# Kernel tuning notes

Hardware: AMD Instinct MI355X
Metric: run time of the kernel (lower is better)

## Reference

```python
import jax, jax.numpy as jnp
import numpy as np

ITEM_NUM = 50000
MAXLEN = 128
D_MODEL = 64
D_STATE = 32
D_CONV = 4
EXPAND = 2
D_INNER = EXPAND * D_MODEL  # 128
DT_RANK = max(1, -(-D_MODEL // 16))  # ceil(64/16) = 4
STD = 0.02


def setup_inputs() -> dict:
    key = jax.random.key(0)
    ks = jax.random.split(key, 12)
    B, L = 32, MAXLEN
    input_ids = jax.random.randint(ks[0], (B, L), 0, ITEM_NUM + 1)
    item_emb = STD * jax.random.normal(ks[1], (ITEM_NUM + 1, D_MODEL), jnp.float32)
    item_emb = item_emb.at[0].set(0.0)  # padding_idx=0 zeroed
    pos_emb = STD * jax.random.normal(ks[2], (MAXLEN, D_MODEL), jnp.float32)
    in_proj_w = STD * jax.random.normal(ks[3], (2 * D_INNER, D_MODEL), jnp.float32)
    conv_w = STD * jax.random.normal(ks[4], (D_INNER, D_CONV), jnp.float32)
    conv_b = jnp.zeros((D_INNER,), jnp.float32)
    x_proj_w = STD * jax.random.normal(ks[5], (DT_RANK + 2 * D_STATE, D_INNER), jnp.float32)
    dt_proj_w = STD * jax.random.normal(ks[6], (D_INNER, DT_RANK), jnp.float32)
    dt_proj_b = jnp.zeros((D_INNER,), jnp.float32)
    # A initialized as log of 1..d_state broadcast over channels (mamba_ssm S4D-real init)
    A_log = jnp.log(jnp.broadcast_to(jnp.arange(1, D_STATE + 1, dtype=jnp.float32), (D_INNER, D_STATE)))
    D_param = jnp.ones((D_INNER,), jnp.float32)
    out_proj_w = STD * jax.random.normal(ks[7], (D_MODEL, D_INNER), jnp.float32)
    return dict(input_ids=input_ids, item_emb=item_emb, pos_emb=pos_emb,
                in_proj_w=in_proj_w, conv_w=conv_w, conv_b=conv_b,
                x_proj_w=x_proj_w, dt_proj_w=dt_proj_w, dt_proj_b=dt_proj_b,
                A_log=A_log, D_param=D_param, out_proj_w=out_proj_w)


def _mamba_block(x, in_proj_w, conv_w, conv_b, x_proj_w, dt_proj_w, dt_proj_b, A_log, D_param, out_proj_w):
    B, L, _ = x.shape
    xz = jnp.einsum('bld,ed->ble', x, in_proj_w)  # (B,L,2*D_INNER)
    xc, z = jnp.split(xz, 2, axis=-1)
    # causal depthwise conv1d, kernel D_CONV, left-pad D_CONV-1
    xp = jnp.pad(xc, ((0, 0), (D_CONV - 1, 0), (0, 0)))
    xc = sum(xp[:, k:k + L, :] * conv_w[:, k] for k in range(D_CONV)) + conv_b
    xc = jax.nn.silu(xc)
    dbl = jnp.einsum('blc,ec->ble', xc, x_proj_w)
    dt, Bm, Cm = jnp.split(dbl, [DT_RANK, DT_RANK + D_STATE], axis=-1)
    delta = jax.nn.softplus(jnp.einsum('blr,cr->blc', dt, dt_proj_w) + dt_proj_b)  # (B,L,D_INNER)
    A = -jnp.exp(A_log)  # (D_INNER, D_STATE)
    dA = jnp.exp(delta[..., None] * A)                       # (B,L,C,S)
    dBu = delta[..., None] * Bm[:, :, None, :] * xc[..., None]  # (B,L,C,S)

    def step(h, inp):
        dA_t, dBu_t, C_t = inp  # (B,C,S),(B,C,S),(B,S)
        h = dA_t * h + dBu_t
        y = jnp.einsum('bcs,bs->bc', h, C_t)
        return h, y

    h0 = jnp.zeros((B, D_INNER, D_STATE), xc.dtype)
    _, ys = jax.lax.scan(step, h0, (dA.transpose(1, 0, 2, 3), dBu.transpose(1, 0, 2, 3), Cm.transpose(1, 0, 2)))
    y = ys.transpose(1, 0, 2) + D_param * xc  # (B,L,D_INNER)
    y = y * jax.nn.silu(z)
    return jnp.einsum('blc,dc->bld', y, out_proj_w)


def reference(input_ids, item_emb, pos_emb, in_proj_w, conv_w, conv_b,
              x_proj_w, dt_proj_w, dt_proj_b, A_log, D_param, out_proj_w):
    B, L = input_ids.shape
    seqs = item_emb[input_ids] * (D_MODEL ** 0.5)
    seqs = seqs + pos_emb[jnp.arange(L)][None, :, :]
    # dropout is identity in eval/deterministic mode
    pad_mask = (input_ids == 0)
    seqs = jnp.where(pad_mask[..., None], 0.0, seqs)
    seqs = _mamba_block(seqs, in_proj_w, conv_w, conv_b, x_proj_w,
                        dt_proj_w, dt_proj_b, A_log, D_param, out_proj_w)
    logits = jnp.einsum('bld,vd->blv', seqs, item_emb)  # matmul with item_emb.T
    return logits
```

## Files before the change

kernel.cpp:

```cpp
#include <hip/hip_runtime.h>
#include <math.h>

#define BB 32
#define LL 128
#define DM 64
#define DI 128
#define NV 50001
#define BL (BB*LL)
#define TM 32
#define TN 512
#define NT2 98
#define NPAD2 (NT2*TN)

typedef float f32x4 __attribute__((ext_vector_type(4)));
typedef _Float16 h16x8 __attribute__((ext_vector_type(8)));

__device__ __forceinline__ float silu_f(float x) { return x / (1.0f + expf(-x)); }

__global__ __launch_bounds__(512, 1) void k_pre(
    const int* __restrict__ ids, const float* __restrict__ item_emb,
    const float* __restrict__ pos_emb, const float* __restrict__ in_proj_w,
    const float* __restrict__ conv_w, const float* __restrict__ conv_b,
    const float* __restrict__ x_proj_w, const float* __restrict__ dt_proj_w,
    const float* __restrict__ dt_proj_b,
    float* __restrict__ zs_g, float* __restrict__ xcs_g,
    float* __restrict__ dbl_g, float* __restrict__ delta_g) {
    __shared__ float sq[67 * 68];
    __shared__ float px[67 * 132];
    __shared__ float cvS[64 * 132];
    __shared__ float dblS[64 * 68];
    const int t = threadIdx.x;
    const int bb = blockIdx.x >> 1, half = blockIdx.x & 1;
    const int l0 = half * 64;

    {
        int d = t & 63;
        for (int i = t >> 6; i < 67; i += 8) {
            int tl = l0 - 3 + i;
            float v = 0.f;
            if (tl >= 0) {
                int id = ids[bb * LL + tl];
                if (id != 0) v = item_emb[id * DM + d] * 8.0f + pos_emb[tl * DM + d];
            }
            sq[i * 68 + d] = v;
        }
    }
    __syncthreads();
    {
        int r = t & 63;
        int q = __builtin_amdgcn_readfirstlane(t >> 6);
        f32x4 s4[16];
        #pragma unroll
        for (int k = 0; k < 16; k++) s4[k] = *(const f32x4*)&sq[r * 68 + 4 * k];
        float acc[32];
        #pragma unroll
        for (int j = 0; j < 32; j++) acc[j] = 0.f;
        const float* wq = in_proj_w + (q * 32) * DM;
        #pragma unroll 4
        for (int j = 0; j < 32; j++) {
            float a = 0.f;
            #pragma unroll
            for (int k = 0; k < 16; k++) {
                f32x4 w4 = *(const f32x4*)&wq[j * DM + 4 * k];
                a += s4[k].x * w4.x + s4[k].y * w4.y + s4[k].z * w4.z + s4[k].w * w4.w;
            }
            acc[j] = a;
        }
        int tok = l0 - 3 + r;
        if (q < 4) {
            #pragma unroll
            for (int j4 = 0; j4 < 8; j4++) {
                f32x4 v = {acc[4 * j4], acc[4 * j4 + 1], acc[4 * j4 + 2], acc[4 * j4 + 3]};
                *(f32x4*)&px[r * 132 + q * 32 + 4 * j4] = v;
            }
        } else if (tok >= 0) {
            float* dst = zs_g + (size_t)(bb * LL + tok) * DI + (q - 4) * 32;
            #pragma unroll
            for (int j = 0; j < 32; j++) dst[j] = silu_f(acc[j]);
        }
    }
    __syncthreads();
    {
        int e = t & 255;
        for (int hr = 64 + (t >> 8); hr < 67; hr += 2) {
            float a = 0.f;
            const float* w = in_proj_w + e * DM;
            #pragma unroll
            for (int k = 0; k < 16; k++) {
                f32x4 sv = *(const f32x4*)&sq[hr * 68 + 4 * k];
                f32x4 wv = *(const f32x4*)&w[4 * k];
                a += sv.x * wv.x + sv.y * wv.y + sv.z * wv.z + sv.w * wv.w;
            }
            int tok = l0 - 3 + hr;
            if (e < 128) px[hr * 132 + e] = a;
            else zs_g[(size_t)(bb * LL + tok) * DI + (e - 128)] = silu_f(a);
        }
    }
    __syncthreads();
    {
        int c = t & 127, r4 = t >> 7;
        float cw0 = conv_w[c * 4], cw1 = conv_w[c * 4 + 1];
        float cw2 = conv_w[c * 4 + 2], cw3 = conv_w[c * 4 + 3];
        float cb = conv_b[c];
        for (int g = 0; g < 16; g++) {
            int j = 4 * g + r4;
            float x0 = px[j * 132 + c], x1 = px[(j + 1) * 132 + c];
            float x2 = px[(j + 2) * 132 + c], x3 = px[(j + 3) * 132 + c];
            float v = silu_f(cb + x0 * cw0 + x1 * cw1 + x2 * cw2 + x3 * cw3);
            cvS[j * 132 + c] = v;
            xcs_g[(size_t)(bb * LL + l0 + j) * DI + c] = v;
        }
    }
    __syncthreads();
    {
        int r = t & 63;
        int q = __builtin_amdgcn_readfirstlane(t >> 6);
        int e0 = q * 9;
        float acc[9];
        #pragma unroll
        for (int j = 0; j < 9; j++) acc[j] = 0.f;
        #pragma unroll
        for (int kc = 0; kc < 4; kc++) {
            f32x4 xr[8];
            #pragma unroll
            for (int k4 = 0; k4 < 8; k4++)
                xr[k4] = *(const f32x4*)&cvS[r * 132 + kc * 32 + 4 * k4];
            #pragma unroll
            for (int j = 0; j < 9; j++) {
                int e = e0 + j;
                if (e < 68) {
                    const float* w = x_proj_w + (size_t)e * DI + kc * 32;
                    float a = acc[j];
                    #pragma unroll
                    for (int k4 = 0; k4 < 8; k4++) {
                        f32x4 wv = *(const f32x4*)&w[4 * k4];
                        a += xr[k4].x * wv.x + xr[k4].y * wv.y + xr[k4].z * wv.z + xr[k4].w * wv.w;
                    }
                    acc[j] = a;
                }
            }
        }
        int row = bb * LL + l0 + r;
        #pragma unroll
        for (int j = 0; j < 9; j++) {
            int e = e0 + j;
            if (e < 68) {
                dblS[r * 68 + e] = acc[j];
                if (e >= 4) dbl_g[(size_t)row * 64 + (e - 4)] = acc[j];
            }
        }
    }
    __syncthreads();
    {
        int r = t & 63;
        int q = __builtin_amdgcn_readfirstlane(t >> 6);
        f32x4 dt = *(const f32x4*)&dblS[r * 68];
        int row = bb * LL + l0 + r;
        #pragma unroll
        for (int j = 0; j < 16; j++) {
            int c = q * 16 + j;
            float a = dt_proj_b[c] + dt.x * dt_proj_w[c * 4] + dt.y * dt_proj_w[c * 4 + 1]
                    + dt.z * dt_proj_w[c * 4 + 2] + dt.w * dt_proj_w[c * 4 + 3];
            float sp = (a > 20.f) ? a : log1pf(expf(a));
            delta_g[(size_t)row * DI + c] = sp;
        }
    }
}

__global__ __launch_bounds__(512, 1) void k_scan(
    const float* __restrict__ delta_g, const float* __restrict__ xcs_g,
    const float* __restrict__ dbl_g, const float* __restrict__ zs_g,
    const float* __restrict__ A_log, const float* __restrict__ Dp,
    float* __restrict__ y_g) {
    const int t = threadIdx.x;
    const int b = blockIdx.x >> 3, ce = blockIdx.x & 7;
    const int grp = t >> 5, s = t & 31;
    const int c = ce * 16 + grp;
    const size_t r0 = (size_t)(b * LL);
    float Acs = -expf(A_log[c * 32 + s]);
    float Dc = Dp[c];
    float h = 0.f;
    float Bt = dbl_g[r0 * 64 + s], Ct = dbl_g[r0 * 64 + 32 + s];
    float dlt = delta_g[r0 * DI + c], xct = xcs_g[r0 * DI + c];
    float zt = zs_g[r0 * DI + c];
    for (int tt = 0; tt < LL; tt++) {
        float Bn = 0.f, Cn = 0.f, zn = 0.f, dn = 0.f, xn = 0.f;
        if (tt < LL - 1) {
            size_t rn = r0 + tt + 1;
            Bn = dbl_g[rn * 64 + s]; Cn = dbl_g[rn * 64 + 32 + s];
            dn = delta_g[rn * DI + c]; xn = xcs_g[rn * DI + c];
            zn = zs_g[rn * DI + c];
        }
        h = expf(dlt * Acs) * h + (dlt * Bt) * xct;
        float p = h * Ct;
        #pragma unroll
        for (int off = 16; off; off >>= 1) p += __shfl_xor(p, off, 32);
        if (s == 0) y_g[(r0 + tt) * DI + c] = (p + Dc * xct) * zt;
        dlt = dn; xct = xn; Bt = Bn; Ct = Cn; zt = zn;
    }
}

__global__ void k_outproj(const float* __restrict__ y, const float* __restrict__ w,
                          _Float16* __restrict__ outp_h) {
    int row = blockIdx.x;
    int d = threadIdx.x;
    __shared__ float ys[DI];
    ys[d] = y[(size_t)row * DI + d];
    ys[d + 64] = y[(size_t)row * DI + d + 64];
    __syncthreads();
    float acc = 0.f;
    const float* wr = w + d * DI;
    #pragma unroll
    for (int c = 0; c < DI; c++) acc += ys[c] * wr[c];
    outp_h[(size_t)row * 64 + d] = (_Float16)(acc * 262144.0f);
}

__global__ void k_cvt_emb(const float* __restrict__ emb, _Float16* __restrict__ embh) {
    int i = blockIdx.x * 256 + threadIdx.x;
    int r = i >> 6, d = i & 63;
    float v = (r < NV) ? emb[(size_t)r * 64 + d] * 1024.0f : 0.f;
    embh[i] = (_Float16)v;
}

__global__ __launch_bounds__(256, 2) void k_logits(
    const _Float16* __restrict__ A, const _Float16* __restrict__ Bm,
    float* __restrict__ logits) {
    __shared__ _Float16 As[TM * 72];
    __shared__ _Float16 Bs[TN * 72];
    const int m0 = blockIdx.x * TM;
    const int n0 = blockIdx.y * TN;
    const int t = threadIdx.x;

    {
        int r = t >> 3, c8 = t & 7;
        *(h16x8*)&As[r * 72 + c8 * 8] = *(const h16x8*)&A[(size_t)(m0 + r) * 64 + c8 * 8];
    }
    #pragma unroll
    for (int q = 0; q < 16; q++) {
        int idx = t + q * 256;
        int r = idx >> 3, c8 = idx & 7;
        *(h16x8*)&Bs[r * 72 + c8 * 8] = *(const h16x8*)&Bm[(size_t)(n0 + r) * 64 + c8 * 8];
    }
    __syncthreads();

    const int lane = t & 63, wv = t >> 6;
    const int lr = lane & 15, lg = lane >> 4;
    f32x4 acc[2][8];
    #pragma unroll
    for (int mi = 0; mi < 2; mi++)
        #pragma unroll
        for (int ni = 0; ni < 8; ni++)
            acc[mi][ni] = f32x4{0.f, 0.f, 0.f, 0.f};

    #pragma unroll
    for (int step = 0; step < 2; step++) {
        int kb = step * 32 + lg * 8;
        h16x8 a[2], b[8];
        #pragma unroll
        for (int mi = 0; mi < 2; mi++)
            a[mi] = *(const h16x8*)&As[(16 * mi + lr) * 72 + kb];
        #pragma unroll
        for (int ni = 0; ni < 8; ni++)
            b[ni] = *(const h16x8*)&Bs[(128 * wv + 16 * ni + lr) * 72 + kb];
        #pragma unroll
        for (int mi = 0; mi < 2; mi++)
            #pragma unroll
            for (int ni = 0; ni < 8; ni++)
                acc[mi][ni] = __builtin_amdgcn_mfma_f32_16x16x32_f16(a[mi], b[ni], acc[mi][ni], 0, 0, 0);
    }
    __syncthreads();

    float* Cs = (float*)Bs;
    const float SC = 3.7252902984619140625e-09f;
    #pragma unroll
    for (int mi = 0; mi < 2; mi++)
        #pragma unroll
        for (int ni = 0; ni < 8; ni++) {
            int col = 128 * wv + 16 * ni + lr;
            #pragma unroll
            for (int j = 0; j < 4; j++) {
                int row = 16 * mi + 4 * lg + j;
                Cs[row * 517 + col] = acc[mi][ni][j] * SC;
            }
        }
    __syncthreads();

    #pragma unroll
    for (int q = 0; q < 16; q++) {
        int r = 2 * q + (t >> 7);
        int c = t & 127;
        int grow = m0 + r;
        int s = (4 - (grow & 3)) & 3;
        float* dst = logits + (size_t)grow * NV + n0;
        const float* src = Cs + r * 517;
        if (s == 0) {
            int col = 4 * c;
            int gc = n0 + col;
            if (gc + 3 < NV) {
                __builtin_nontemporal_store(*(const f32x4*)&src[col], (f32x4*)&dst[col]);
            } else {
                #pragma unroll
                for (int e = 0; e < 4; e++)
                    if (gc + e < NV) __builtin_nontemporal_store(src[col + e], &dst[col + e]);
            }
        } else {
            if (c == 0) {
                for (int e = 0; e < s; e++)
                    if (n0 + e < NV) __builtin_nontemporal_store(src[e], &dst[e]);
            }
            if (c < 127) {
                int col = s + 4 * c;
                int gc = n0 + col;
                if (gc + 3 < NV) {
                    __builtin_nontemporal_store(*(const f32x4*)&src[col], (f32x4*)&dst[col]);
                } else {
                    #pragma unroll
                    for (int e = 0; e < 4; e++)
                        if (gc + e < NV) __builtin_nontemporal_store(src[col + e], &dst[col + e]);
                }
            } else {
                for (int e = s + 508; e < 512; e++)
                    if (n0 + e < NV) __builtin_nontemporal_store(src[e], &dst[e]);
            }
        }
    }
}

extern "C" void kernel_launch(void* const* d_in, const int* in_sizes, int n_in,
                              void* d_out, int out_size, void* d_ws, size_t ws_size,
                              hipStream_t stream) {
    const int*   ids       = (const int*)  d_in[0];
    const float* item_emb  = (const float*)d_in[1];
    const float* pos_emb   = (const float*)d_in[2];
    const float* in_proj_w = (const float*)d_in[3];
    const float* conv_w    = (const float*)d_in[4];
    const float* conv_b    = (const float*)d_in[5];
    const float* x_proj_w  = (const float*)d_in[6];
    const float* dt_proj_w = (const float*)d_in[7];
    const float* dt_proj_b = (const float*)d_in[8];
    const float* A_log     = (const float*)d_in[9];
    const float* Dp        = (const float*)d_in[10];
    const float* out_proj_w= (const float*)d_in[11];
    float* logits = (float*)d_out;

    float* ws     = (float*)d_ws;
    float* zs     = ws;
    float* xcs    = zs + (size_t)BL * DI;
    float* dblg   = xcs + (size_t)BL * DI;
    float* deltag = dblg + (size_t)BL * 64;
    float* yg     = deltag + (size_t)BL * DI;
    _Float16* outph = (_Float16*)(yg + (size_t)BL * DI);
    _Float16* embh  = outph + (size_t)BL * 64;

    k_cvt_emb<<<(NPAD2 * 64) / 256, 256, 0, stream>>>(item_emb, embh);
    k_pre<<<64, 512, 0, stream>>>(ids, item_emb, pos_emb, in_proj_w, conv_w, conv_b,
                                  x_proj_w, dt_proj_w, dt_proj_b,
                                  zs, xcs, dblg, deltag);
    k_scan<<<256, 512, 0, stream>>>(deltag, xcs, dblg, zs, A_log, Dp, yg);
    k_outproj<<<BL, 64, 0, stream>>>(yg, out_proj_w, outph);
    dim3 lgd(BL / TM, NT2);
    k_logits<<<lgd, 256, 0, stream>>>(outph, embh, logits);
}
```

Before: 412.7 us.

## Split preprocessing into 16-token tiles and batch out-projection rows per block

k_pre now runs 256 blocks, each handling 16 tokens with a 3-token halo, instead of 64 blocks of 64 tokens. The GEMV loops are restructured so each thread keeps a weight row in registers and streams activations from shared memory. k_outproj processes 8 rows per 256-thread block with weights held in registers and vectorised loads, replacing one tiny block per row. The intent is more parallelism across CUs and less launch and weight-reload overhead, at the cost of redundant halo recomputation and higher register pressure.

```diff
diff --git a/kernel.cpp b/kernel.cpp
--- a/kernel.cpp
+++ b/kernel.cpp
@@ -25,18 +25,18 @@
     const float* __restrict__ dt_proj_b,
     float* __restrict__ zs_g, float* __restrict__ xcs_g,
     float* __restrict__ dbl_g, float* __restrict__ delta_g) {
-    __shared__ float sq[67 * 68];
-    __shared__ float px[67 * 132];
-    __shared__ float cvS[64 * 132];
-    __shared__ float dblS[64 * 68];
+    __shared__ float sq[19 * 68];
+    __shared__ float px[19 * 132];
+    __shared__ float cvS[16 * 132];
+    __shared__ float dtS[16 * 4];
     const int t = threadIdx.x;
-    const int bb = blockIdx.x >> 1, half = blockIdx.x & 1;
-    const int l0 = half * 64;
+    const int bb = blockIdx.x >> 3, e8 = blockIdx.x & 7;
+    const int T0 = e8 * 16;
 
     {
         int d = t & 63;
-        for (int i = t >> 6; i < 67; i += 8) {
-            int tl = l0 - 3 + i;
+        for (int i = t >> 6; i < 19; i += 8) {
+            int tl = T0 - 3 + i;
             float v = 0.f;
             if (tl >= 0) {
                 int id = ids[bb * LL + tl];
@@ -47,122 +47,82 @@
     }
     __syncthreads();
     {
-        int r = t & 63;
-        int q = __builtin_amdgcn_readfirstlane(t >> 6);
-        f32x4 s4[16];
-        #pragma unroll
-        for (int k = 0; k < 16; k++) s4[k] = *(const f32x4*)&sq[r * 68 + 4 * k];
-        float acc[32];
-        #pragma unroll
-        for (int j = 0; j < 32; j++) acc[j] = 0.f;
-        const float* wq = in_proj_w + (q * 32) * DM;
-        #pragma unroll 4
-        for (int j = 0; j < 32; j++) {
+        int e = t & 255, half = t >> 8;
+        f32x4 w4[16];
+        const float* wr = in_proj_w + e * DM;
+        #pragma unroll
+        for (int k = 0; k < 16; k++) w4[k] = *(const f32x4*)&wr[4 * k];
+        int i0 = half ? 10 : 0, i1 = half ? 19 : 10;
+        for (int i = i0; i < i1; i++) {
             float a = 0.f;
             #pragma unroll
             for (int k = 0; k < 16; k++) {
-                f32x4 w4 = *(const f32x4*)&wq[j * DM + 4 * k];
-                a += s4[k].x * w4.x + s4[k].y * w4.y + s4[k].z * w4.z + s4[k].w * w4.w;
-            }
-            acc[j] = a;
-        }
-        int tok = l0 - 3 + r;
-        if (q < 4) {
-            #pragma unroll
-            for (int j4 = 0; j4 < 8; j4++) {
-                f32x4 v = {acc[4 * j4], acc[4 * j4 + 1], acc[4 * j4 + 2], acc[4 * j4 + 3]};
-                *(f32x4*)&px[r * 132 + q * 32 + 4 * j4] = v;
-            }
-        } else if (tok >= 0) {
-            float* dst = zs_g + (size_t)(bb * LL + tok) * DI + (q - 4) * 32;
-            #pragma unroll
-            for (int j = 0; j < 32; j++) dst[j] = silu_f(acc[j]);
-        }
-    }
-    __syncthreads();
-    {
-        int e = t & 255;
-        for (int hr = 64 + (t >> 8); hr < 67; hr += 2) {
-            float a = 0.f;
-            const float* w = in_proj_w + e * DM;
-            #pragma unroll
-            for (int k = 0; k < 16; k++) {
-                f32x4 sv = *(const f32x4*)&sq[hr * 68 + 4 * k];
-                f32x4 wv = *(const f32x4*)&w[4 * k];
-                a += sv.x * wv.x + sv.y * wv.y + sv.z * wv.z + sv.w * wv.w;
-            }
-            int tok = l0 - 3 + hr;
-            if (e < 128) px[hr * 132 + e] = a;
-            else zs_g[(size_t)(bb * LL + tok) * DI + (e - 128)] = silu_f(a);
-        }
-    }
-    __syncthreads();
-    {
-        int c = t & 127, r4 = t >> 7;
+                f32x4 s = *(const f32x4*)&sq[i * 68 + 4 * k];
+                a += s.x * w4[k].x + s.y * w4[k].y + s.z * w4[k].z + s.w * w4[k].w;
+            }
+            if (e < 128) px[i * 132 + e] = a;
+            else if (i >= 3) zs_g[(size_t)(bb * LL + T0 + i - 3) * DI + (e - 128)] = silu_f(a);
+        }
+    }
+    __syncthreads();
+    {
+        int c = t & 127;
         float cw0 = conv_w[c * 4], cw1 = conv_w[c * 4 + 1];
         float cw2 = conv_w[c * 4 + 2], cw3 = conv_w[c * 4 + 3];
         float cb = conv_b[c];
-        for (int g = 0; g < 16; g++) {
-            int j = 4 * g + r4;
-            float x0 = px[j * 132 + c], x1 = px[(j + 1) * 132 + c];
-            float x2 = px[(j + 2) * 132 + c], x3 = px[(j + 3) * 132 + c];
-            float v = silu_f(cb + x0 * cw0 + x1 * cw1 + x2 * cw2 + x3 * cw3);
+        #pragma unroll
+        for (int m = 0; m < 4; m++) {
+            int j = 4 * m + (t >> 7);
+            float v = silu_f(cb + px[j * 132 + c] * cw0 + px[(j + 1) * 132 + c] * cw1
+                                + px[(j + 2) * 132 + c] * cw2 + px[(j + 3) * 132 + c] * cw3);
             cvS[j * 132 + c] = v;
-            xcs_g[(size_t)(bb * LL + l0 + j) * DI + c] = v;
-        }
-    }
-    __syncthreads();
-    {
-        int r = t & 63;
-        int q = __builtin_amdgcn_readfirstlane(t >> 6);
-        int e0 = q * 9;
-        float acc[9];
-        #pragma unroll
-        for (int j = 0; j < 9; j++) acc[j] = 0.f;
-        #pragma unroll
-        for (int kc = 0; kc < 4; kc++) {
-            f32x4 xr[8];
-            #pragma unroll
-            for (int k4 = 0; k4 < 8; k4++)
-                xr[k4] = *(const f32x4*)&cvS[r * 132 + kc * 32 + 4 * k4];
-            #pragma unroll
-            for (int j = 0; j < 9; j++) {
-                int e = e0 + j;
-                if (e < 68) {
-                    const float* w = x_proj_w + (size_t)e * DI + kc * 32;
-                    float a = acc[j];
-                    #pragma unroll
-                    for (int k4 = 0; k4 < 8; k4++) {
-                        f32x4 wv = *(const f32x4*)&w[4 * k4];
-                        a += xr[k4].x * wv.x + xr[k4].y * wv.y + xr[k4].z * wv.z + xr[k4].w * wv.w;
-                    }
-                    acc[j] = a;
-                }
-            }
-        }
-        int row = bb * LL + l0 + r;
-        #pragma unroll
-        for (int j = 0; j < 9; j++) {
-            int e = e0 + j;
-            if (e < 68) {
-                dblS[r * 68 + e] = acc[j];
-                if (e >= 4) dbl_g[(size_t)row * 64 + (e - 4)] = acc[j];
-            }
-        }
-    }
-    __syncthreads();
-    {
-        int r = t & 63;
-        int q = __builtin_amdgcn_readfirstlane(t >> 6);
-        f32x4 dt = *(const f32x4*)&dblS[r * 68];
-        int row = bb * LL + l0 + r;
-        #pragma unroll
-        for (int j = 0; j < 16; j++) {
-            int c = q * 16 + j;
-            float a = dt_proj_b[c] + dt.x * dt_proj_w[c * 4] + dt.y * dt_proj_w[c * 4 + 1]
-                    + dt.z * dt_proj_w[c * 4 + 2] + dt.w * dt_proj_w[c * 4 + 3];
+            xcs_g[(size_t)(bb * LL + T0 + j) * DI + c] = v;
+        }
+    }
+    __syncthreads();
+    {
+        int e = 4 + (t & 63), jg = t >> 6;
+        f32x4 w4[32];
+        const float* wr = x_proj_w + (size_t)e * DI;
+        #pragma unroll
+        for (int k = 0; k < 32; k++) w4[k] = *(const f32x4*)&wr[4 * k];
+        #pragma unroll
+        for (int jj = 0; jj < 2; jj++) {
+            int j = jg + 8 * jj;
+            float a = 0.f;
+            #pragma unroll
+            for (int k = 0; k < 32; k++) {
+                f32x4 x = *(const f32x4*)&cvS[j * 132 + 4 * k];
+                a += x.x * w4[k].x + x.y * w4[k].y + x.z * w4[k].z + x.w * w4[k].w;
+            }
+            dbl_g[(size_t)(bb * LL + T0 + j) * 64 + (e - 4)] = a;
+        }
+        if (t < 64) {
+            int j2 = t >> 2, e2 = t & 3;
+            const float* wr2 = x_proj_w + (size_t)e2 * DI;
+            float a = 0.f;
+            #pragma unroll
+            for (int k = 0; k < 32; k++) {
+                f32x4 x = *(const f32x4*)&cvS[j2 * 132 + 4 * k];
+                f32x4 w2 = *(const f32x4*)&wr2[4 * k];
+                a += x.x * w2.x + x.y * w2.y + x.z * w2.z + x.w * w2.w;
+            }
+            dtS[j2 * 4 + e2] = a;
+        }
+    }
+    __syncthreads();
+    {
+        int c = t & 127;
+        float dw0 = dt_proj_w[c * 4], dw1 = dt_proj_w[c * 4 + 1];
+        float dw2 = dt_proj_w[c * 4 + 2], dw3 = dt_proj_w[c * 4 + 3];
+        float db = dt_proj_b[c];
+        #pragma unroll
+        for (int m = 0; m < 4; m++) {
+            int j = 4 * m + (t >> 7);
+            float a = db + dtS[j * 4] * dw0 + dtS[j * 4 + 1] * dw1
+                         + dtS[j * 4 + 2] * dw2 + dtS[j * 4 + 3] * dw3;
             float sp = (a > 20.f) ? a : log1pf(expf(a));
-            delta_g[(size_t)row * DI + c] = sp;
+            delta_g[(size_t)(bb * LL + T0 + j) * DI + c] = sp;
         }
     }
 }
@@ -200,19 +160,33 @@
     }
 }
 
-__global__ void k_outproj(const float* __restrict__ y, const float* __restrict__ w,
-                          _Float16* __restrict__ outp_h) {
-    int row = blockIdx.x;
-    int d = threadIdx.x;
-    __shared__ float ys[DI];
-    ys[d] = y[(size_t)row * DI + d];
-    ys[d + 64] = y[(size_t)row * DI + d + 64];
-    __syncthreads();
-    float acc = 0.f;
+__global__ __launch_bounds__(256, 2) void k_outproj(
+    const float* __restrict__ y, const float* __restrict__ w,
+    _Float16* __restrict__ outp_h) {
+    __shared__ float ys[8 * 132];
+    const int t = threadIdx.x;
+    const int r0 = blockIdx.x * 8;
+    {
+        int r = t >> 5, c4 = t & 31;
+        *(f32x4*)&ys[r * 132 + 4 * c4] = *(const f32x4*)&y[(size_t)(r0 + r) * DI + 4 * c4];
+    }
+    __syncthreads();
+    int d = t & 63, rh = t >> 6;
+    f32x4 w4[32];
     const float* wr = w + d * DI;
     #pragma unroll
-    for (int c = 0; c < DI; c++) acc += ys[c] * wr[c];
-    outp_h[(size_t)row * 64 + d] = (_Float16)(acc * 262144.0f);
+    for (int k = 0; k < 32; k++) w4[k] = *(const f32x4*)&wr[4 * k];
+    #pragma unroll
+    for (int jj = 0; jj < 2; jj++) {
+        int r = rh + 4 * jj;
+        float a = 0.f;
+        #pragma unroll
+        for (int k = 0; k < 32; k++) {
+            f32x4 x = *(const f32x4*)&ys[r * 132 + 4 * k];
+            a += x.x * w4[k].x + x.y * w4[k].y + x.z * w4[k].z + x.w * w4[k].w;
+        }
+        outp_h[(size_t)(r0 + r) * 64 + d] = (_Float16)(a * 262144.0f);
+    }
 }
 
 __global__ void k_cvt_emb(const float* __restrict__ emb, _Float16* __restrict__ embh) {
@@ -353,11 +327,11 @@
     _Float16* embh  = outph + (size_t)BL * 64;
 
     k_cvt_emb<<<(NPAD2 * 64) / 256, 256, 0, stream>>>(item_emb, embh);
-    k_pre<<<64, 512, 0, stream>>>(ids, item_emb, pos_emb, in_proj_w, conv_w, conv_b,
-                                  x_proj_w, dt_proj_w, dt_proj_b,
-                                  zs, xcs, dblg, deltag);
+    k_pre<<<256, 512, 0, stream>>>(ids, item_emb, pos_emb, in_proj_w, conv_w, conv_b,
+                                   x_proj_w, dt_proj_w, dt_proj_b,
+                                   zs, xcs, dblg, deltag);
     k_scan<<<256, 512, 0, stream>>>(deltag, xcs, dblg, zs, A_log, Dp, yg);
-    k_outproj<<<BL, 64, 0, stream>>>(yg, out_proj_w, outph);
+    k_outproj<<<BL / 8, 256, 0, stream>>>(yg, out_proj_w, outph);
     dim3 lgd(BL / TM, NT2);
     k_logits<<<lgd, 256, 0, stream>>>(outph, embh, logits);
 }
```

Result: faster. 366.2 us (median of 2 runs) (-11.3%).
